# Optimization experiments

Measured on AMD Instinct MI355X. Metric: run time of the kernel, lower is better.

The kernel has to match this reference:

```python
import jax, jax.numpy as jnp
import numpy as np

N_EMBD = 768
HIDDEN = 4 * N_EMBD
N_EXPERTS = 8
TOP_K = 2


def setup_inputs() -> dict:
    key = jax.random.key(0)
    ks = jax.random.split(key, 4)
    B, T, C, E, H = 4, 2048, N_EMBD, N_EXPERTS, HIDDEN
    x = jax.random.normal(ks[0], (B, T, C), dtype=jnp.float32)
    gate_w = jax.random.normal(ks[1], (E, C), dtype=jnp.float32) * 0.02
    gate_b = jnp.zeros((E,), dtype=jnp.float32)
    w_fc = jax.random.normal(ks[2], (E, H, C), dtype=jnp.float32) * 0.02
    b_fc = jnp.zeros((E, H), dtype=jnp.float32)
    w_proj = jax.random.normal(ks[3], (E, C, H), dtype=jnp.float32) * 0.02
    b_proj = jnp.zeros((E, C), dtype=jnp.float32)
    return {"x": x, "gate_w": gate_w, "gate_b": gate_b, "w_fc": w_fc,
            "b_fc": b_fc, "w_proj": w_proj, "b_proj": b_proj}


def reference(x, gate_w, gate_b, w_fc, b_fc, w_proj, b_proj):
    B, T, C = x.shape
    E = gate_b.shape[0]
    xf = x.reshape(-1, C)  # [N, C]
    # gating: Linear(C -> E), top-k, softmax over the k selected scores
    scores = xf @ gate_w.T + gate_b                      # [N, E]
    top_s, top_i = jax.lax.top_k(scores, TOP_K)          # [N, K]
    gates = jax.nn.softmax(top_s, axis=-1)               # [N, K]
    # combine weight per (token, expert): sum_k gate[t,k] * 1[top_i[t,k]==e]
    comb = jnp.sum(jax.nn.one_hot(top_i, E, dtype=xf.dtype) * gates[..., None], axis=1)  # [N, E]
    out = jnp.zeros_like(xf)
    for j in range(E):  # loop over fixed small expert count
        h = jax.nn.gelu(xf @ w_fc[j].T + b_fc[j], approximate=True)  # [N, H]
        y = h @ w_proj[j].T + b_proj[j]                              # [N, C]
        out = out + comb[:, j:j + 1] * y
    return out.reshape(B, T, C)
```

## Files before the change

### kernel.cpp

```cpp
#include <hip/hip_runtime.h>
#include <cmath>

#define N_TOK 8192
#define C_DIM 768
#define H_DIM 3072
#define NEXP  8
#define PADCAP 17408
#define MAXMT  136

typedef short short8 __attribute__((ext_vector_type(8)));
typedef float f32x4  __attribute__((ext_vector_type(4)));

__device__ __forceinline__ unsigned short f2b(float f) {
  unsigned int u = __float_as_uint(f);
  u += 0x7fffu + ((u >> 16) & 1u);
  return (unsigned short)(u >> 16);
}
__device__ __forceinline__ float b2f(unsigned short u) {
  return __uint_as_float((unsigned int)u << 16);
}
__device__ __forceinline__ void gll(const char* g, char* l) {
  __builtin_amdgcn_global_load_lds((const __attribute__((address_space(1))) void*)g,
                                   (__attribute__((address_space(3))) void*)l, 16, 0, 0);
}

__global__ __launch_bounds__(256) void gate_kernel(
    const float* __restrict__ x, const float* __restrict__ gw,
    const float* __restrict__ gb, int* __restrict__ counts,
    int* __restrict__ tok_e, int* __restrict__ tok_r, float* __restrict__ tok_w) {
  __shared__ float gwl[NEXP * C_DIM];
  __shared__ double red[256][NEXP];
  int tid = threadIdx.x;
  const float4* gw4 = (const float4*)gw;
  float4* gl4 = (float4*)gwl;
  for (int i = tid; i < NEXP * C_DIM / 4; i += 256) gl4[i] = gw4[i];
  __syncthreads();
  int tl = tid & 63;
  int kc = tid >> 6;
  int t = blockIdx.x * 64 + tl;
  double acc[NEXP];
#pragma unroll
  for (int e = 0; e < NEXP; e++) acc[e] = 0.0;
  const float* xr = x + (size_t)t * C_DIM;
  for (int k = kc * 192; k < kc * 192 + 192; k++) {
    double xv = (double)xr[k];
#pragma unroll
    for (int e = 0; e < NEXP; e++) acc[e] += xv * (double)gwl[e * C_DIM + k];
  }
#pragma unroll
  for (int e = 0; e < NEXP; e++) red[tid][e] = acc[e];
  __syncthreads();
  if (tid < 64) {
    double s[NEXP];
#pragma unroll
    for (int e = 0; e < NEXP; e++)
      s[e] = (double)gb[e] + red[tid][e] + red[tid + 64][e] + red[tid + 128][e] + red[tid + 192][e];
    double best = s[0], sec = -1e300; int bi = 0, si = -1;
#pragma unroll
    for (int e = 1; e < NEXP; e++) {
      if (s[e] > best)      { sec = best; si = bi; best = s[e]; bi = e; }
      else if (s[e] > sec)  { sec = s[e]; si = e; }
    }
    double ex = exp(sec - best);
    double den = 1.0 + ex;
    tok_e[2 * t] = bi;  tok_e[2 * t + 1] = si;
    tok_w[2 * t] = (float)(1.0 / den);  tok_w[2 * t + 1] = (float)(ex / den);
    tok_r[2 * t]     = atomicAdd(&counts[bi], 1);
    tok_r[2 * t + 1] = atomicAdd(&counts[si], 1);
  }
}

__global__ void offsets_kernel(const int* __restrict__ counts, int* __restrict__ po) {
  if (threadIdx.x == 0 && blockIdx.x == 0) {
    int s = 0;
    for (int e = 0; e < NEXP; e++) { po[e] = s; s += (counts[e] + 127) & ~127; }
    po[NEXP] = s;
  }
}

__global__ __launch_bounds__(256) void scatter_kernel(
    const int* __restrict__ tok_e, const int* __restrict__ tok_r,
    const float* __restrict__ tok_w, const int* __restrict__ po,
    int* __restrict__ perm_t, float* __restrict__ perm_w,
    int* __restrict__ tok_pos) {
  int t = blockIdx.x * 256 + threadIdx.x;
#pragma unroll
  for (int k = 0; k < 2; k++) {
    int e = tok_e[2 * t + k];
    int pos = po[e] + tok_r[2 * t + k];
    perm_t[pos] = t;
    perm_w[pos] = tok_w[2 * t + k];
    tok_pos[2 * t + k] = pos;
  }
}

__global__ __launch_bounds__(256) void gather_kernel(
    const float* __restrict__ x, const int* __restrict__ po,
    const int* __restrict__ perm_t, unsigned short* __restrict__ xg) {
  int row = blockIdx.x * 4 + (threadIdx.x >> 6);
  if (row >= po[NEXP]) return;
  int l = threadIdx.x & 63;
  int t = perm_t[row];
  const float4* src = (const float4*)(x + (size_t)t * C_DIM);
  ushort4* dst = (ushort4*)(xg + (size_t)row * C_DIM);
#pragma unroll
  for (int j = 0; j < 3; j++) {
    float4 v = src[l + j * 64];
    ushort4 o; o.x = f2b(v.x); o.y = f2b(v.y); o.z = f2b(v.z); o.w = f2b(v.w);
    dst[l + j * 64] = o;
  }
}

__global__ __launch_bounds__(256) void wconv_kernel(
    const float* __restrict__ wfc, const float* __restrict__ wproj,
    unsigned short* __restrict__ wfcb, unsigned short* __restrict__ wpjb) {
  const int n4 = NEXP * H_DIM * C_DIM / 4;
  int stride = gridDim.x * blockDim.x;
  for (int i = blockIdx.x * blockDim.x + threadIdx.x; i < 2 * n4; i += stride) {
    const float4* s; ushort4* d; int j;
    if (i < n4) { s = (const float4*)wfc;   d = (ushort4*)wfcb; j = i; }
    else        { s = (const float4*)wproj; d = (ushort4*)wpjb; j = i - n4; }
    float4 v = s[j];
    ushort4 o; o.x = f2b(v.x); o.y = f2b(v.y); o.z = f2b(v.z); o.w = f2b(v.w);
    d[j] = o;
  }
}

__device__ __forceinline__ void gemm_core512(
    const unsigned short* A, int lda, const unsigned short* B, int ldb, int K,
    char* lds, int tid, f32x4 acc[4][2]) {
  const int w = tid >> 6, l = tid & 63;
  const int wr = w >> 2, wc = w & 3;
  const int rowa = wr * 64 + (l & 15);
  const int rowb = wc * 32 + (l & 15);
  const int kc = l >> 4;
  const int sa0 = (kc ^ ((rowa >> 1) & 7)) * 16;
  const int sb0 = (kc ^ ((rowb >> 1) & 7)) * 16;
  const int r0 = tid >> 3,          cg0 = (tid & 7) ^ ((r0 >> 1) & 7);
  const int r1 = (512 + tid) >> 3,  cg1 = ((512 + tid) & 7) ^ ((r1 >> 1) & 7);
  const char* gA0 = (const char*)(A + (size_t)r0 * lda) + cg0 * 16;
  const char* gA1 = (const char*)(A + (size_t)r1 * lda) + cg1 * 16;
  const char* gB0 = (const char*)(B + (size_t)r0 * ldb) + cg0 * 16;
  const char* gB1 = (const char*)(B + (size_t)r1 * ldb) + cg1 * 16;
  const int wb = w * 1024;
  const int iters = K >> 6;
  gll(gA0, lds + wb);
  gll(gA1, lds + 8192 + wb);
  gll(gB0, lds + 16384 + wb);
  gll(gB1, lds + 24576 + wb);
#pragma unroll 1
  for (int kt = 0; kt < iters; kt++) {
    __syncthreads();
    if (kt + 1 < iters) {
      size_t kb = (size_t)(kt + 1) * 128;
      char* nb = lds + ((kt + 1) & 1) * 32768;
      gll(gA0 + kb, nb + wb);
      gll(gA1 + kb, nb + 8192 + wb);
      gll(gB0 + kb, nb + 16384 + wb);
      gll(gB1 + kb, nb + 24576 + wb);
    }
    char* bb = lds + (kt & 1) * 32768;
#pragma unroll
    for (int s = 0; s < 2; s++) {
      const int sxa = sa0 ^ (s << 6);
      const int sxb = sb0 ^ (s << 6);
      short8 af[4], bf2[2];
#pragma unroll
      for (int mi = 0; mi < 4; mi++)
        af[mi] = *(const short8*)(bb + (rowa + mi * 16) * 128 + sxa);
#pragma unroll
      for (int ni = 0; ni < 2; ni++)
        bf2[ni] = *(const short8*)(bb + 16384 + (rowb + ni * 16) * 128 + sxb);
#pragma unroll
      for (int mi = 0; mi < 4; mi++)
#pragma unroll
        for (int ni = 0; ni < 2; ni++)
          acc[mi][ni] = __builtin_amdgcn_mfma_f32_16x16x32_bf16(af[mi], bf2[ni], acc[mi][ni], 0, 0, 0);
    }
  }
}

__global__ __launch_bounds__(512, 4) void fc1_kernel(
    const unsigned short* __restrict__ xg, const unsigned short* __restrict__ wfcb,
    const float* __restrict__ bfc, const int* __restrict__ po,
    unsigned short* __restrict__ h) {
  __shared__ char lds[65536];
  int bid = blockIdx.x;
  int r8 = bid & 7, g8 = bid >> 3;
  int col = g8 % 24;
  int Sp  = g8 / 24;
  int y   = r8 * 17 + Sp;
  int row0 = y * 128;
  if (row0 >= po[NEXP]) return;
  int e = 0;
#pragma unroll
  for (int i = 1; i < NEXP; i++) if (row0 >= po[i]) e = i;
  int n0 = col * 128;
  int tid = threadIdx.x;
  f32x4 acc[4][2];
#pragma unroll
  for (int mi = 0; mi < 4; mi++)
#pragma unroll
    for (int ni = 0; ni < 2; ni++) acc[mi][ni] = (f32x4){0.f, 0.f, 0.f, 0.f};
  gemm_core512(xg + (size_t)row0 * C_DIM, C_DIM,
               wfcb + (size_t)e * H_DIM * C_DIM + (size_t)n0 * C_DIM, C_DIM, C_DIM,
               lds, tid, acc);
  int w = tid >> 6, l = tid & 63;
  int wr = w >> 2, wc = w & 3, q = l >> 4;
  const float* bias = bfc + (size_t)e * H_DIM;
#pragma unroll
  for (int ni = 0; ni < 2; ni++) {
    int colw = n0 + wc * 32 + ni * 16 + (l & 15);
    float bv = bias[colw];
#pragma unroll
    for (int mi = 0; mi < 4; mi++) {
#pragma unroll
      for (int r = 0; r < 4; r++) {
        int row = row0 + wr * 64 + mi * 16 + q * 4 + r;
        float v = acc[mi][ni][r] + bv;
        float g = 0.5f * v * (1.0f + tanhf(0.7978845608028654f * (v + 0.044715f * v * v * v)));
        h[(size_t)row * H_DIM + colw] = f2b(g);
      }
    }
  }
}

__global__ __launch_bounds__(512, 4) void fc2_kernel(
    const unsigned short* __restrict__ h, const unsigned short* __restrict__ wpjb,
    const float* __restrict__ bproj, const int* __restrict__ po,
    const float* __restrict__ perm_w, unsigned short* __restrict__ part) {
  __shared__ char lds[65536];
  int bid = blockIdx.x;
  int r8 = bid & 7, g8 = bid >> 3;
  int col = g8 % 6;
  int Sp  = g8 / 6;
  int S   = r8 * 34 + Sp;
  int z   = S / 136;
  int y   = S - z * 136;
  int row0 = y * 128;
  if (row0 >= po[NEXP]) return;
  int e = 0;
#pragma unroll
  for (int i = 1; i < NEXP; i++) if (row0 >= po[i]) e = i;
  int n0 = col * 128;
  int koff = z * (H_DIM / 2);
  int tid = threadIdx.x;
  f32x4 acc[4][2];
#pragma unroll
  for (int mi = 0; mi < 4; mi++)
#pragma unroll
    for (int ni = 0; ni < 2; ni++) acc[mi][ni] = (f32x4){0.f, 0.f, 0.f, 0.f};
  gemm_core512(h + (size_t)row0 * H_DIM + koff, H_DIM,
               wpjb + (size_t)e * C_DIM * H_DIM + (size_t)n0 * H_DIM + koff, H_DIM, H_DIM / 2,
               lds, tid, acc);
  int w = tid >> 6, l = tid & 63;
  int wr = w >> 2, wc = w & 3, q = l >> 4;
  const float* bias = bproj + (size_t)e * C_DIM;
  unsigned short* pz = part + (size_t)z * PADCAP * C_DIM;
#pragma unroll
  for (int mi = 0; mi < 4; mi++) {
#pragma unroll
    for (int r = 0; r < 4; r++) {
      int pos = row0 + wr * 64 + mi * 16 + q * 4 + r;
      float wgt = perm_w[pos];
#pragma unroll
      for (int ni = 0; ni < 2; ni++) {
        int colw = n0 + wc * 32 + ni * 16 + (l & 15);
        float v = acc[mi][ni][r];
        if (z == 0) v += bias[colw];
        pz[(size_t)pos * C_DIM + colw] = f2b(v * wgt);
      }
    }
  }
}

__global__ __launch_bounds__(256) void combine_kernel(
    const unsigned short* __restrict__ part, const int* __restrict__ tok_pos,
    float* __restrict__ out) {
  const int NC4 = C_DIM / 4;
  int idx = blockIdx.x * 256 + threadIdx.x;
  int t = idx / NC4, c4 = idx - t * NC4;
  int p0 = tok_pos[2 * t], p1 = tok_pos[2 * t + 1];
  const size_t SP = (size_t)PADCAP * C_DIM;
  const unsigned short* r00 = part + (size_t)p0 * C_DIM + c4 * 4;
  const unsigned short* r10 = part + (size_t)p1 * C_DIM + c4 * 4;
  ushort4 v00 = *(const ushort4*)r00;
  ushort4 v01 = *(const ushort4*)(r00 + SP);
  ushort4 v10 = *(const ushort4*)r10;
  ushort4 v11 = *(const ushort4*)(r10 + SP);
  float4 o;
  o.x = b2f(v00.x) + b2f(v01.x) + b2f(v10.x) + b2f(v11.x);
  o.y = b2f(v00.y) + b2f(v01.y) + b2f(v10.y) + b2f(v11.y);
  o.z = b2f(v00.z) + b2f(v01.z) + b2f(v10.z) + b2f(v11.z);
  o.w = b2f(v00.w) + b2f(v01.w) + b2f(v10.w) + b2f(v11.w);
  ((float4*)out)[idx] = o;
}

extern "C" void kernel_launch(void* const* d_in, const int* in_sizes, int n_in,
                              void* d_out, int out_size, void* d_ws, size_t ws_size,
                              hipStream_t stream) {
  const float* x     = (const float*)d_in[0];
  const float* gw    = (const float*)d_in[1];
  const float* gb    = (const float*)d_in[2];
  const float* wfc   = (const float*)d_in[3];
  const float* bfc   = (const float*)d_in[4];
  const float* wproj = (const float*)d_in[5];
  const float* bproj = (const float*)d_in[6];
  float* out = (float*)d_out;
  char* ws = (char*)d_ws;

  int*   counts  = (int*)(ws + 0);
  int*   po      = (int*)(ws + 64);
  int*   tok_e   = (int*)(ws + 256);
  int*   tok_r   = (int*)(ws + 65792);
  float* tok_w   = (float*)(ws + 131328);
  int*   tok_pos = (int*)(ws + 196864);
  int*   perm_t  = (int*)(ws + 262400);
  float* perm_w  = (float*)(ws + 332032);
  const size_t ROUT_END = 401920;
  unsigned short* wpjb = (unsigned short*)(ws + 401920);
  unsigned short* hbuf = (unsigned short*)(ws + 38150656);
  unsigned short* xg   = (unsigned short*)(ws + 145105408);
  unsigned short* wfcb = (unsigned short*)(ws + 171844096);
  unsigned short* part = (unsigned short*)(ws + 145105408);

  hipMemsetAsync(ws, 0, ROUT_END, stream);

  gate_kernel<<<N_TOK / 64, 256, 0, stream>>>(x, gw, gb, counts, tok_e, tok_r, tok_w);
  offsets_kernel<<<1, 64, 0, stream>>>(counts, po);
  scatter_kernel<<<N_TOK / 256, 256, 0, stream>>>(tok_e, tok_r, tok_w, po, perm_t, perm_w, tok_pos);
  gather_kernel<<<PADCAP / 4, 256, 0, stream>>>(x, po, perm_t, xg);
  wconv_kernel<<<2048, 256, 0, stream>>>(wfc, wproj, wfcb, wpjb);
  fc1_kernel<<<8 * 17 * 24, 512, 0, stream>>>(xg, wfcb, bfc, po, hbuf);
  fc2_kernel<<<8 * 34 * 6, 512, 0, stream>>>(hbuf, wpjb, bproj, po, perm_w, part);
  combine_kernel<<<N_TOK * (C_DIM / 4) / 256, 256, 0, stream>>>(part, tok_pos, out);
}
```

Before: 531.9 us.

## Use fast GELU, nontemporal memory ops, and simpler LDS address math in MoE kernels

Replaces the tanhf GELU with an algebraically equivalent sigmoid form built on the hardware exp2 and reciprocal intrinsics. Marks streaming loads and stores in the weight conversion, fc1/fc2 epilogues and combine kernel as nontemporal to cut cache pollution. Precomputes the swizzled LDS fragment offsets and advances the global pointers incrementally in the GEMM inner loop to reduce integer work. The fast exp and reciprocal trade a little accuracy for speed, and nontemporal stores of h could hurt reuse if fc2 would otherwise hit in cache.

New measurement: 557.6 us. +4.8%, slower.

```diff
diff --git a/kernel.cpp b/kernel.cpp
--- a/kernel.cpp
+++ b/kernel.cpp
@@ -10,6 +10,8 @@
 
 typedef short short8 __attribute__((ext_vector_type(8)));
 typedef float f32x4  __attribute__((ext_vector_type(4)));
+typedef unsigned short us4 __attribute__((ext_vector_type(4)));
+typedef float fl4 __attribute__((ext_vector_type(4)));
 
 __device__ __forceinline__ unsigned short f2b(float f) {
   unsigned int u = __float_as_uint(f);
@@ -22,6 +24,12 @@
 __device__ __forceinline__ void gll(const char* g, char* l) {
   __builtin_amdgcn_global_load_lds((const __attribute__((address_space(1))) void*)g,
                                    (__attribute__((address_space(3))) void*)l, 16, 0, 0);
+}
+__device__ __forceinline__ float gelu_f(float v) {
+  float u = v * v;
+  float p = __builtin_fmaf(u, 0.044715f * v, v);
+  float e = __builtin_amdgcn_exp2f(p * -2.3022084f);
+  return v * __builtin_amdgcn_rcpf(1.0f + e);
 }
 
 __global__ __launch_bounds__(256) void gate_kernel(
@@ -117,11 +125,11 @@
   const int n4 = NEXP * H_DIM * C_DIM / 4;
   int stride = gridDim.x * blockDim.x;
   for (int i = blockIdx.x * blockDim.x + threadIdx.x; i < 2 * n4; i += stride) {
-    const float4* s; ushort4* d; int j;
-    if (i < n4) { s = (const float4*)wfc;   d = (ushort4*)wfcb; j = i; }
-    else        { s = (const float4*)wproj; d = (ushort4*)wpjb; j = i - n4; }
-    float4 v = s[j];
-    ushort4 o; o.x = f2b(v.x); o.y = f2b(v.y); o.z = f2b(v.z); o.w = f2b(v.w);
+    const fl4* s; us4* d; int j;
+    if (i < n4) { s = (const fl4*)wfc;   d = (us4*)wfcb; j = i; }
+    else        { s = (const fl4*)wproj; d = (us4*)wpjb; j = i - n4; }
+    fl4 v = __builtin_nontemporal_load(&s[j]);
+    us4 o; o.x = f2b(v.x); o.y = f2b(v.y); o.z = f2b(v.z); o.w = f2b(v.w);
     d[j] = o;
   }
 }
@@ -134,8 +142,8 @@
   const int rowa = wr * 64 + (l & 15);
   const int rowb = wc * 32 + (l & 15);
   const int kc = l >> 4;
-  const int sa0 = (kc ^ ((rowa >> 1) & 7)) * 16;
-  const int sb0 = (kc ^ ((rowb >> 1) & 7)) * 16;
+  const int aoff = rowa * 128 + (kc ^ ((rowa >> 1) & 7)) * 16;
+  const int boff = 16384 + rowb * 128 + (kc ^ ((rowb >> 1) & 7)) * 16;
   const int r0 = tid >> 3,          cg0 = (tid & 7) ^ ((r0 >> 1) & 7);
   const int r1 = (512 + tid) >> 3,  cg1 = ((512 + tid) & 7) ^ ((r1 >> 1) & 7);
   const char* gA0 = (const char*)(A + (size_t)r0 * lda) + cg0 * 16;
@@ -152,25 +160,28 @@
   for (int kt = 0; kt < iters; kt++) {
     __syncthreads();
     if (kt + 1 < iters) {
-      size_t kb = (size_t)(kt + 1) * 128;
+      gA0 += 128; gA1 += 128; gB0 += 128; gB1 += 128;
       char* nb = lds + ((kt + 1) & 1) * 32768;
-      gll(gA0 + kb, nb + wb);
-      gll(gA1 + kb, nb + 8192 + wb);
-      gll(gB0 + kb, nb + 16384 + wb);
-      gll(gB1 + kb, nb + 24576 + wb);
-    }
-    char* bb = lds + (kt & 1) * 32768;
+      gll(gA0, nb + wb);
+      gll(gA1, nb + 8192 + wb);
+      gll(gB0, nb + 16384 + wb);
+      gll(gB1, nb + 24576 + wb);
+    }
+    const char* bb = lds + (kt & 1) * 32768;
 #pragma unroll
     for (int s = 0; s < 2; s++) {
-      const int sxa = sa0 ^ (s << 6);
-      const int sxb = sb0 ^ (s << 6);
+      const int sx = s << 6;
       short8 af[4], bf2[2];
 #pragma unroll
-      for (int mi = 0; mi < 4; mi++)
-        af[mi] = *(const short8*)(bb + (rowa + mi * 16) * 128 + sxa);
-#pragma unroll
-      for (int ni = 0; ni < 2; ni++)
-        bf2[ni] = *(const short8*)(bb + 16384 + (rowb + ni * 16) * 128 + sxb);
+      for (int mi = 0; mi < 4; mi++) {
+        int o = aoff + mi * 2048;
+        af[mi] = *(const short8*)(bb + ((o & ~127) | ((o & 127) ^ sx)));
+      }
+#pragma unroll
+      for (int ni = 0; ni < 2; ni++) {
+        int o = boff + ni * 2048;
+        bf2[ni] = *(const short8*)(bb + ((o & ~127) | ((o & 127) ^ sx)));
+      }
 #pragma unroll
       for (int mi = 0; mi < 4; mi++)
 #pragma unroll
@@ -217,9 +228,8 @@
 #pragma unroll
       for (int r = 0; r < 4; r++) {
         int row = row0 + wr * 64 + mi * 16 + q * 4 + r;
-        float v = acc[mi][ni][r] + bv;
-        float g = 0.5f * v * (1.0f + tanhf(0.7978845608028654f * (v + 0.044715f * v * v * v)));
-        h[(size_t)row * H_DIM + colw] = f2b(g);
+        float g = gelu_f(acc[mi][ni][r] + bv);
+        __builtin_nontemporal_store(f2b(g), &h[(size_t)row * H_DIM + colw]);
       }
     }
   }
@@ -268,7 +278,7 @@
         int colw = n0 + wc * 32 + ni * 16 + (l & 15);
         float v = acc[mi][ni][r];
         if (z == 0) v += bias[colw];
-        pz[(size_t)pos * C_DIM + colw] = f2b(v * wgt);
+        __builtin_nontemporal_store(f2b(v * wgt), &pz[(size_t)pos * C_DIM + colw]);
       }
     }
   }
@@ -284,16 +294,16 @@
   const size_t SP = (size_t)PADCAP * C_DIM;
   const unsigned short* r00 = part + (size_t)p0 * C_DIM + c4 * 4;
   const unsigned short* r10 = part + (size_t)p1 * C_DIM + c4 * 4;
-  ushort4 v00 = *(const ushort4*)r00;
-  ushort4 v01 = *(const ushort4*)(r00 + SP);
-  ushort4 v10 = *(const ushort4*)r10;
-  ushort4 v11 = *(const ushort4*)(r10 + SP);
-  float4 o;
+  us4 v00 = __builtin_nontemporal_load((const us4*)r00);
+  us4 v01 = __builtin_nontemporal_load((const us4*)(r00 + SP));
+  us4 v10 = __builtin_nontemporal_load((const us4*)r10);
+  us4 v11 = __builtin_nontemporal_load((const us4*)(r10 + SP));
+  fl4 o;
   o.x = b2f(v00.x) + b2f(v01.x) + b2f(v10.x) + b2f(v11.x);
   o.y = b2f(v00.y) + b2f(v01.y) + b2f(v10.y) + b2f(v11.y);
   o.z = b2f(v00.z) + b2f(v01.z) + b2f(v10.z) + b2f(v11.z);
   o.w = b2f(v00.w) + b2f(v01.w) + b2f(v10.w) + b2f(v11.w);
-  ((float4*)out)[idx] = o;
+  __builtin_nontemporal_store(o, &((fl4*)out)[idx]);
 }
 
 extern "C" void kernel_launch(void* const* d_in, const int* in_sizes, int n_in,
```
